# Kernel tuning notes

Measured on AMD Instinct MI355X. Metric: run time of the kernel, lower is better.

## Reference

```python
import jax, jax.numpy as jnp
import numpy as np

B, D, U = 4096, 1024, 1024

def cumax(a):
    # Faithful to source: softmax over last axis, cumsum over axis 0 (TF defaults).
    return jnp.cumsum(jax.nn.softmax(a, axis=-1), axis=0)

def setup_inputs() -> dict:
    key = jax.random.key(0)
    ks = jax.random.split(key, 21)
    names = ['inputs', 'hidden_prev', 'cell_prev',
             'Wf', 'Uf', 'bf', 'Wi', 'Ui', 'bi', 'Wo', 'Uo', 'bo',
             'Wc', 'Uc', 'bc', 'Wft', 'Uft', 'bft', 'Wit', 'Uit', 'bit']
    shapes = [(B, D), (B, U), (B, U)] + [(D, U), (U, U), (U,)] * 6
    scales = [1.0, 1.0, 1.0] + [0.05, 0.05, 0.05] * 6  # random_normal init ~ small stddev
    return {n: jax.random.normal(k, s, dtype=jnp.float32) * sc
            for n, k, s, sc in zip(names, ks, shapes, scales)}

def reference(inputs, hidden_prev, cell_prev,
              Wf, Uf, bf, Wi, Ui, bi, Wo, Uo, bo,
              Wc, Uc, bc, Wft, Uft, bft, Wit, Uit, bit):
    # Fuse the 12 small GEMMs into 2 big ones: [B,D]@[D,6U] and [B,U]@[U,6U]
    W_all = jnp.concatenate([Wf, Wi, Wo, Wc, Wft, Wit], axis=1)   # [D, 6U]
    U_all = jnp.concatenate([Uf, Ui, Uo, Uc, Uft, Uit], axis=1)   # [U, 6U]
    b_all = jnp.concatenate([bf, bi, bo, bc, bft, bit], axis=0)   # [6U]
    pre = inputs @ W_all + hidden_prev @ U_all + b_all            # [B, 6U]
    zf, zi, zo, zc, zft, zit = [pre[:, j*U:(j+1)*U] for j in range(6)]

    f = jax.nn.sigmoid(zf)
    i = jax.nn.sigmoid(zi)
    o = jax.nn.sigmoid(zo)
    c_hat = jnp.tanh(zc)
    f_tilde = cumax(zft)
    i_tilde = 1.0 - cumax(zit)

    omega = f_tilde * i_tilde
    f_hat = f * omega + (f_tilde - omega)
    i_hat = i * omega + (i_tilde - omega)
    cell = f_hat * cell_prev + i_hat * c_hat
    hidden = o * jnp.tanh(cell)
    return hidden, cell
```

## Files before the change

kernel.cpp:

```cpp
#include <hip/hip_runtime.h>
#include <cstdint>
#include <cstddef>


typedef _Float16 half8  __attribute__((ext_vector_type(8)));
typedef _Float16 half4v __attribute__((ext_vector_type(4)));
typedef float f32x4 __attribute__((ext_vector_type(4)));

__device__ __forceinline__ void async16(const _Float16* g, _Float16* l) {
  __builtin_amdgcn_global_load_lds(
      (const __attribute__((address_space(1))) void*)g,
      (__attribute__((address_space(3))) void*)l, 16, 0, 0);
}

struct Ptrs12 { const float* p[12]; };
struct Ptrs6  { const float* p[6];  };

__global__ void prep(const float* __restrict__ X, const float* __restrict__ H,
                     Ptrs12 w, Ptrs6 bs,
                     _Float16* __restrict__ Ahi, _Float16* __restrict__ Bhi,
                     float* __restrict__ b_all) {
  __shared__ float tile[64][65];
  const int blk = blockIdx.x;
  const int t = threadIdx.x;
  if (blk < 8192) {
    size_t base = ((size_t)blk * 256 + t) * 4;
    int k = (int)(base & 2047);
    size_t b = base >> 11;
    const float* src = (k < 1024) ? (X + b * 1024 + k) : (H + b * 1024 + (k - 1024));
    float4 v = *(const float4*)src;
    half4v hi = { (_Float16)v.x, (_Float16)v.y, (_Float16)v.z, (_Float16)v.w };
    *(half4v*)(Ahi + base) = hi;
  } else if (blk < 11264) {
    int bb = blk - 8192;
    int mat = bb >> 8;
    int tl = bb & 255;
    int tr = tl >> 4, tc = tl & 15;
    int g = mat >> 1, s = mat & 1;
    const float* src = w.p[mat];
    int col = t & 63, r0 = t >> 6;
#pragma unroll
    for (int i = 0; i < 16; i++) {
      int row = i * 4 + r0;
      tile[row][col] = src[(size_t)(tr * 64 + row) * 1024 + tc * 64 + col];
    }
    __syncthreads();
    int c2 = t >> 2, kseg = t & 3;
    half8 v0, v1;
#pragma unroll
    for (int j = 0; j < 8; j++) {
      v0[j] = (_Float16)(tile[kseg * 16 + j][c2] * 64.0f);
      v1[j] = (_Float16)(tile[kseg * 16 + 8 + j][c2] * 64.0f);
    }
    size_t n  = (size_t)g * 1024 + tc * 64 + c2;
    size_t kk = (size_t)s * 1024 + tr * 64 + kseg * 16;
    *(half8*)(Bhi + n * 2048 + kk) = v0;
    *(half8*)(Bhi + n * 2048 + kk + 8) = v1;
  } else {
    int n = (blk - 11264) * 256 + t;
    b_all[n] = bs.p[n >> 10][n & 1023];
  }
}


#define LGKM0 asm volatile("s_waitcnt lgkmcnt(0)" ::: "memory")

__device__ __forceinline__ void wg_barrier() {
  __builtin_amdgcn_s_barrier();
  asm volatile("" ::: "memory");
}

__global__ __launch_bounds__(512, 2) void gemm_ring(
    const _Float16* __restrict__ Ah, const _Float16* __restrict__ Bh,
    const float* __restrict__ b_all, _Float16* __restrict__ pre16) {
  __shared__ __attribute__((aligned(16))) _Float16 lds[73728];

  const int bid = blockIdx.x;
  const int swz = (bid & 7) * 96 + (bid >> 3);
  const int nTile = swz / 32;
  const int mTile = swz % 32;

  const int t = threadIdx.x;
  const int lane = t & 63;
  const int wave = t >> 6;
  const int wm = wave >> 2, wn = wave & 3;
  const int kgrp = lane >> 4, frow = lane & 15;

  const _Float16* Abase = Ah + (size_t)mTile * 128 * 2048;
  const _Float16* Bbase = Bh + (size_t)nTile * 256 * 2048;

  f32x4 acc[4][4] = {};

  auto stage_tile = [&](int kt, int base) {
#pragma unroll
    for (int q = 0; q < 2; q++) {
      int s = q * 512 + t;
      int r = s >> 3, k8 = s & 7;
      int xs = k8 ^ (r & 7);
      async16(Abase + (size_t)r * 2048 + kt * 64 + xs * 8, lds + base + s * 8);
    }
#pragma unroll
    for (int q = 0; q < 4; q++) {
      int s = q * 512 + t;
      int r = s >> 3, k8 = s & 7;
      int xs = k8 ^ (r & 7);
      async16(Bbase + (size_t)r * 2048 + kt * 64 + xs * 8,
              lds + base + 8192 + s * 8);
    }
  };

  int cur = 0, nxt = 24576, nn = 49152;

  stage_tile(0, cur);
  stage_tile(1, nxt);
  asm volatile("s_waitcnt vmcnt(6)" ::: "memory");
  wg_barrier();

  for (int T = 0; T < 32; T++) {
    const _Float16* A_ = lds + cur;
    const _Float16* B_ = lds + cur + 8192;
    half8 af[4][2], bf[4][2];
#pragma unroll
    for (int mi = 0; mi < 4; mi++) {
      int r = wm * 64 + mi * 16 + frow;
#pragma unroll
      for (int ks = 0; ks < 2; ks++)
        af[mi][ks] = *(const half8*)(A_ + r * 64 +
                                     (((ks * 4 + kgrp) ^ (r & 7)) * 8));
    }
#pragma unroll
    for (int nj = 0; nj < 4; nj++) {
      int r = wn * 64 + nj * 16 + frow;
#pragma unroll
      for (int ks = 0; ks < 2; ks++)
        bf[nj][ks] = *(const half8*)(B_ + r * 64 +
                                     (((ks * 4 + kgrp) ^ (r & 7)) * 8));
    }
    if (T + 2 < 32) stage_tile(T + 2, nn);

    __builtin_amdgcn_s_setprio(1);
#pragma unroll
    for (int mi = 0; mi < 4; mi++)
#pragma unroll
      for (int nj = 0; nj < 4; nj++)
        acc[mi][nj] = __builtin_amdgcn_mfma_f32_16x16x32_f16(
            af[mi][0], bf[nj][0], acc[mi][nj], 0, 0, 0);
    __builtin_amdgcn_s_setprio(0);

    LGKM0;
    if (T < 30) {
      asm volatile("s_waitcnt vmcnt(6)" ::: "memory");
      wg_barrier();
    } else if (T == 30) {
      asm volatile("s_waitcnt vmcnt(0)" ::: "memory");
      wg_barrier();
    }

    __builtin_amdgcn_s_setprio(1);
#pragma unroll
    for (int mi = 0; mi < 4; mi++)
#pragma unroll
      for (int nj = 0; nj < 4; nj++)
        acc[mi][nj] = __builtin_amdgcn_mfma_f32_16x16x32_f16(
            af[mi][1], bf[nj][1], acc[mi][nj], 0, 0, 0);
    __builtin_amdgcn_s_setprio(0);

    int tmp = cur; cur = nxt; nxt = nn; nn = tmp;
  }

  __syncthreads();
  const float inv64 = 1.0f / 64.0f;
  const int cb = nTile * 256;
  float bias[4];
#pragma unroll
  for (int nj = 0; nj < 4; nj++)
    bias[nj] = b_all[cb + wn * 64 + nj * 16 + frow];
#pragma unroll
  for (int mi = 0; mi < 4; mi++) {
#pragma unroll
    for (int nj = 0; nj < 4; nj++) {
      int row = wm * 64 + mi * 16 + kgrp * 4;
      int col = wn * 64 + nj * 16 + frow;
#pragma unroll
      for (int j = 0; j < 4; j++)
        lds[(row + j) * 264 + col] =
            (_Float16)(acc[mi][nj][j] * inv64 + bias[nj]);
    }
  }
  __syncthreads();
#pragma unroll
  for (int rr = 0; rr < 8; rr++) {
    int L = rr * 4096 + t * 8;
    int row = L >> 8, col = L & 255;
    half8 v = *(const half8*)(lds + row * 264 + col);
    *(half8*)(pre16 + (size_t)(mTile * 128 + row) * 6144 + cb + col) = v;
  }
}

__global__ void softmax_partials(_Float16* __restrict__ pre16, f32x4* __restrict__ part4) {
  __shared__ float wsum[4][1024];
  int m = blockIdx.x >> 10;
  int ch = blockIdx.x & 1023;
  int t = threadIdx.x;
  int wave = t >> 6, lane = t & 63;
  f32x4 colacc[4] = {};
  {
    int b = ch * 4 + wave;
    _Float16* row = pre16 + (size_t)b * 6144 + (4 + m) * 1024;
    f32x4 v[4];
    float mx = -3.4e38f;
#pragma unroll
    for (int j = 0; j < 4; j++) {
      half4v h = *(const half4v*)(row + lane * 4 + 256 * j);
      v[j] = f32x4{ (float)h[0], (float)h[1], (float)h[2], (float)h[3] };
      mx = fmaxf(mx, fmaxf(fmaxf(v[j][0], v[j][1]), fmaxf(v[j][2], v[j][3])));
    }
#pragma unroll
    for (int off = 32; off > 0; off >>= 1) mx = fmaxf(mx, __shfl_xor(mx, off, 64));
    float sum = 0.f;
#pragma unroll
    for (int j = 0; j < 4; j++)
#pragma unroll
      for (int q = 0; q < 4; q++) { v[j][q] = __expf(v[j][q] - mx); sum += v[j][q]; }
#pragma unroll
    for (int off = 32; off > 0; off >>= 1) sum += __shfl_xor(sum, off, 64);
    float inv = 1.f / sum;
#pragma unroll
    for (int j = 0; j < 4; j++) {
      v[j] *= inv;
      half4v h = { (_Float16)v[j][0], (_Float16)v[j][1], (_Float16)v[j][2], (_Float16)v[j][3] };
      *(half4v*)(row + lane * 4 + 256 * j) = h;
      colacc[j] += v[j];
    }
  }
#pragma unroll
  for (int j = 0; j < 4; j++)
    *(f32x4*)(&wsum[wave][lane * 4 + 256 * j]) = colacc[j];
  __syncthreads();
  f32x4 s = *(const f32x4*)(&wsum[0][t * 4]);
  s += *(const f32x4*)(&wsum[1][t * 4]);
  s += *(const f32x4*)(&wsum[2][t * 4]);
  s += *(const f32x4*)(&wsum[3][t * 4]);
  part4[((size_t)m * 256 + t) * 1024 + ch] = s;
}

__global__ void scan_partials(const f32x4* __restrict__ part4, f32x4* __restrict__ off4) {
  int gidx = blockIdx.x * 4 + (threadIdx.x >> 6);
  int lane = threadIdx.x & 63;
  size_t base = (size_t)gidx * 1024;
  f32x4 v[16];
  f32x4 s = {};
#pragma unroll
  for (int j = 0; j < 16; j++) {
    v[j] = part4[base + lane * 16 + j];
    s += v[j];
  }
  f32x4 incl = s;
#pragma unroll
  for (int off = 1; off < 64; off <<= 1) {
    f32x4 o;
#pragma unroll
    for (int q = 0; q < 4; q++) o[q] = __shfl_up(incl[q], off, 64);
    if (lane >= off) incl += o;
  }
  f32x4 run = incl - s;
#pragma unroll
  for (int j = 0; j < 16; j++) {
    off4[base + lane * 16 + j] = run;
    run += v[j];
  }
}

__device__ __forceinline__ float fast_sigmoid(float x) {
  return __builtin_amdgcn_rcpf(1.f + __expf(-x));
}
__device__ __forceinline__ float fast_tanh(float x) {
  float xc = fminf(fmaxf(x, -15.f), 15.f);
  float e = __expf(2.f * xc);
  return (e - 1.f) * __builtin_amdgcn_rcpf(e + 1.f);
}

__global__ void onlstm_final(const _Float16* __restrict__ pre16,
                             const float* __restrict__ cprev, const f32x4* __restrict__ off4,
                             float* __restrict__ out) {
  int ch = blockIdx.x;
  int c4 = threadIdx.x;
  int c = c4 * 4;
  f32x4 runf = off4[(size_t)c4 * 1024 + ch];
  f32x4 runi = off4[(size_t)(256 + c4) * 1024 + ch];
  for (int r = 0; r < 4; r++) {
    int b = ch * 4 + r;
    const _Float16* row = pre16 + (size_t)b * 6144;
    half4v zf = *(const half4v*)(row + c);
    half4v zi = *(const half4v*)(row + 1024 + c);
    half4v zo = *(const half4v*)(row + 2048 + c);
    half4v zc = *(const half4v*)(row + 3072 + c);
    half4v pf = *(const half4v*)(row + 4096 + c);
    half4v pi = *(const half4v*)(row + 5120 + c);
    f32x4 cp = *(const f32x4*)(cprev + (size_t)b * 1024 + c);
    f32x4 hid, cel;
#pragma unroll
    for (int q = 0; q < 4; q++) {
      runf[q] += (float)pf[q];
      runi[q] += (float)pi[q];
      float ft = runf[q], it = 1.f - runi[q];
      float f  = fast_sigmoid((float)zf[q]);
      float ii = fast_sigmoid((float)zi[q]);
      float o  = fast_sigmoid((float)zo[q]);
      float chat = fast_tanh((float)zc[q]);
      float omega = ft * it;
      float fhat = f * omega + (ft - omega);
      float ihat = ii * omega + (it - omega);
      float cell = fhat * cp[q] + ihat * chat;
      hid[q] = o * fast_tanh(cell);
      cel[q] = cell;
    }
    *(f32x4*)(out + (size_t)b * 1024 + c) = hid;
    *(f32x4*)(out + (size_t)4194304 + (size_t)b * 1024 + c) = cel;
  }
}

extern "C" void kernel_launch(void* const* d_in, const int* in_sizes, int n_in,
                              void* d_out, int out_size, void* d_ws, size_t ws_size,
                              hipStream_t stream) {
  const float* X = (const float*)d_in[0];
  const float* H = (const float*)d_in[1];
  const float* C = (const float*)d_in[2];

  char* ws = (char*)d_ws;
  _Float16* pre16 = (_Float16*)(ws);
  _Float16* Ahi   = (_Float16*)(ws + 50331648);
  _Float16* Bhi   = (_Float16*)(ws + 67108864);
  float*    b_all = (float*)(ws + 92274688);
  f32x4*    part4 = (f32x4*)(ws + 50331648);
  f32x4*    off4  = (f32x4*)(ws + 58720256);

  Ptrs12 w;
  for (int g = 0; g < 6; g++) {
    w.p[2 * g]     = (const float*)d_in[3 + 3 * g];
    w.p[2 * g + 1] = (const float*)d_in[4 + 3 * g];
  }
  Ptrs6 bs;
  for (int g = 0; g < 6; g++) bs.p[g] = (const float*)d_in[5 + 3 * g];

  prep<<<11288, 256, 0, stream>>>(X, H, w, bs, Ahi, Bhi, b_all);
  gemm_ring<<<768, 512, 0, stream>>>(Ahi, Bhi, b_all, pre16);
  softmax_partials<<<2048, 256, 0, stream>>>(pre16, part4);
  scan_partials<<<128, 256, 0, stream>>>(part4, off4);
  onlstm_final<<<1024, 256, 0, stream>>>(pre16, C, off4, (float*)d_out);
}
```

Baseline: 316.3 us.

## Fuse softmax, scan and final gating into one cooperative kernel with grid sync

Replaces the three tail kernels (softmax partials, partial scan, final elementwise) with a single cooperative kernel of 512 blocks that uses grid.sync between phases. Each block handles 8 rows and keeps the normalized softmax probabilities in LDS instead of writing them back to global and re-reading them, and the scan is restructured to one block per column group. This removes two launches and a global round-trip of the softmax output. In exchange it adds two grid-wide barriers, and the 8-row batch with a 48KB LDS footprint could lower occupancy.

```diff
diff --git a/kernel.cpp b/kernel.cpp
--- a/kernel.cpp
+++ b/kernel.cpp
@@ -1,6 +1,9 @@
 #include <hip/hip_runtime.h>
+#include <hip/hip_cooperative_groups.h>
 #include <cstdint>
 #include <cstddef>
+
+namespace cg = cooperative_groups;
 
 
 typedef _Float16 half8  __attribute__((ext_vector_type(8)));
@@ -197,79 +200,6 @@
   }
 }
 
-__global__ void softmax_partials(_Float16* __restrict__ pre16, f32x4* __restrict__ part4) {
-  __shared__ float wsum[4][1024];
-  int m = blockIdx.x >> 10;
-  int ch = blockIdx.x & 1023;
-  int t = threadIdx.x;
-  int wave = t >> 6, lane = t & 63;
-  f32x4 colacc[4] = {};
-  {
-    int b = ch * 4 + wave;
-    _Float16* row = pre16 + (size_t)b * 6144 + (4 + m) * 1024;
-    f32x4 v[4];
-    float mx = -3.4e38f;
-#pragma unroll
-    for (int j = 0; j < 4; j++) {
-      half4v h = *(const half4v*)(row + lane * 4 + 256 * j);
-      v[j] = f32x4{ (float)h[0], (float)h[1], (float)h[2], (float)h[3] };
-      mx = fmaxf(mx, fmaxf(fmaxf(v[j][0], v[j][1]), fmaxf(v[j][2], v[j][3])));
-    }
-#pragma unroll
-    for (int off = 32; off > 0; off >>= 1) mx = fmaxf(mx, __shfl_xor(mx, off, 64));
-    float sum = 0.f;
-#pragma unroll
-    for (int j = 0; j < 4; j++)
-#pragma unroll
-      for (int q = 0; q < 4; q++) { v[j][q] = __expf(v[j][q] - mx); sum += v[j][q]; }
-#pragma unroll
-    for (int off = 32; off > 0; off >>= 1) sum += __shfl_xor(sum, off, 64);
-    float inv = 1.f / sum;
-#pragma unroll
-    for (int j = 0; j < 4; j++) {
-      v[j] *= inv;
-      half4v h = { (_Float16)v[j][0], (_Float16)v[j][1], (_Float16)v[j][2], (_Float16)v[j][3] };
-      *(half4v*)(row + lane * 4 + 256 * j) = h;
-      colacc[j] += v[j];
-    }
-  }
-#pragma unroll
-  for (int j = 0; j < 4; j++)
-    *(f32x4*)(&wsum[wave][lane * 4 + 256 * j]) = colacc[j];
-  __syncthreads();
-  f32x4 s = *(const f32x4*)(&wsum[0][t * 4]);
-  s += *(const f32x4*)(&wsum[1][t * 4]);
-  s += *(const f32x4*)(&wsum[2][t * 4]);
-  s += *(const f32x4*)(&wsum[3][t * 4]);
-  part4[((size_t)m * 256 + t) * 1024 + ch] = s;
-}
-
-__global__ void scan_partials(const f32x4* __restrict__ part4, f32x4* __restrict__ off4) {
-  int gidx = blockIdx.x * 4 + (threadIdx.x >> 6);
-  int lane = threadIdx.x & 63;
-  size_t base = (size_t)gidx * 1024;
-  f32x4 v[16];
-  f32x4 s = {};
-#pragma unroll
-  for (int j = 0; j < 16; j++) {
-    v[j] = part4[base + lane * 16 + j];
-    s += v[j];
-  }
-  f32x4 incl = s;
-#pragma unroll
-  for (int off = 1; off < 64; off <<= 1) {
-    f32x4 o;
-#pragma unroll
-    for (int q = 0; q < 4; q++) o[q] = __shfl_up(incl[q], off, 64);
-    if (lane >= off) incl += o;
-  }
-  f32x4 run = incl - s;
-#pragma unroll
-  for (int j = 0; j < 16; j++) {
-    off4[base + lane * 16 + j] = run;
-    run += v[j];
-  }
-}
 
 __device__ __forceinline__ float fast_sigmoid(float x) {
   return __builtin_amdgcn_rcpf(1.f + __expf(-x));
@@ -280,43 +210,133 @@
   return (e - 1.f) * __builtin_amdgcn_rcpf(e + 1.f);
 }
 
-__global__ void onlstm_final(const _Float16* __restrict__ pre16,
-                             const float* __restrict__ cprev, const f32x4* __restrict__ off4,
-                             float* __restrict__ out) {
-  int ch = blockIdx.x;
-  int c4 = threadIdx.x;
-  int c = c4 * 4;
-  f32x4 runf = off4[(size_t)c4 * 1024 + ch];
-  f32x4 runi = off4[(size_t)(256 + c4) * 1024 + ch];
-  for (int r = 0; r < 4; r++) {
-    int b = ch * 4 + r;
-    const _Float16* row = pre16 + (size_t)b * 6144;
-    half4v zf = *(const half4v*)(row + c);
-    half4v zi = *(const half4v*)(row + 1024 + c);
-    half4v zo = *(const half4v*)(row + 2048 + c);
-    half4v zc = *(const half4v*)(row + 3072 + c);
-    half4v pf = *(const half4v*)(row + 4096 + c);
-    half4v pi = *(const half4v*)(row + 5120 + c);
-    f32x4 cp = *(const f32x4*)(cprev + (size_t)b * 1024 + c);
-    f32x4 hid, cel;
-#pragma unroll
-    for (int q = 0; q < 4; q++) {
-      runf[q] += (float)pf[q];
-      runi[q] += (float)pi[q];
-      float ft = runf[q], it = 1.f - runi[q];
-      float f  = fast_sigmoid((float)zf[q]);
-      float ii = fast_sigmoid((float)zi[q]);
-      float o  = fast_sigmoid((float)zo[q]);
-      float chat = fast_tanh((float)zc[q]);
-      float omega = ft * it;
-      float fhat = f * omega + (ft - omega);
-      float ihat = ii * omega + (it - omega);
-      float cell = fhat * cp[q] + ihat * chat;
-      hid[q] = o * fast_tanh(cell);
-      cel[q] = cell;
-    }
-    *(f32x4*)(out + (size_t)b * 1024 + c) = hid;
-    *(f32x4*)(out + (size_t)4194304 + (size_t)b * 1024 + c) = cel;
+__global__ __launch_bounds__(256) void fused_tail(
+    const _Float16* __restrict__ pre16, const float* __restrict__ cprev,
+    f32x4* __restrict__ part4, f32x4* __restrict__ off4,
+    float* __restrict__ out) {
+  __shared__ _Float16 p_lds[8 * 2048];
+  __shared__ float wsum[4][1024];
+  __shared__ f32x4 wtot[4];
+
+  cg::grid_group grid = cg::this_grid();
+
+  const int ch = blockIdx.x;
+  const int t = threadIdx.x;
+  const int wave = t >> 6, lane = t & 63;
+
+#pragma unroll
+  for (int m = 0; m < 2; m++) {
+    f32x4 colacc[4] = {};
+#pragma unroll
+    for (int rr = 0; rr < 2; rr++) {
+      int rloc = wave * 2 + rr;
+      int b = ch * 8 + rloc;
+      const _Float16* row = pre16 + (size_t)b * 6144 + (4 + m) * 1024;
+      f32x4 v[4];
+      float mx = -3.4e38f;
+#pragma unroll
+      for (int j = 0; j < 4; j++) {
+        half4v h = *(const half4v*)(row + lane * 4 + 256 * j);
+        v[j] = f32x4{ (float)h[0], (float)h[1], (float)h[2], (float)h[3] };
+        mx = fmaxf(mx, fmaxf(fmaxf(v[j][0], v[j][1]), fmaxf(v[j][2], v[j][3])));
+      }
+#pragma unroll
+      for (int off = 32; off > 0; off >>= 1) mx = fmaxf(mx, __shfl_xor(mx, off, 64));
+      float sum = 0.f;
+#pragma unroll
+      for (int j = 0; j < 4; j++)
+#pragma unroll
+        for (int q = 0; q < 4; q++) { v[j][q] = __expf(v[j][q] - mx); sum += v[j][q]; }
+#pragma unroll
+      for (int off = 32; off > 0; off >>= 1) sum += __shfl_xor(sum, off, 64);
+      float inv = 1.f / sum;
+#pragma unroll
+      for (int j = 0; j < 4; j++) {
+        v[j] *= inv;
+        half4v h = { (_Float16)v[j][0], (_Float16)v[j][1],
+                     (_Float16)v[j][2], (_Float16)v[j][3] };
+        *(half4v*)(&p_lds[rloc * 2048 + m * 1024 + lane * 4 + 256 * j]) = h;
+        colacc[j] += v[j];
+      }
+    }
+#pragma unroll
+    for (int j = 0; j < 4; j++)
+      *(f32x4*)(&wsum[wave][lane * 4 + 256 * j]) = colacc[j];
+    __syncthreads();
+    f32x4 s = *(const f32x4*)(&wsum[0][t * 4]);
+    s += *(const f32x4*)(&wsum[1][t * 4]);
+    s += *(const f32x4*)(&wsum[2][t * 4]);
+    s += *(const f32x4*)(&wsum[3][t * 4]);
+    part4[((size_t)m * 256 + t) * 512 + ch] = s;
+    __syncthreads();
+  }
+
+  __threadfence();
+  grid.sync();
+  __threadfence();
+
+  {
+    const int g = ch;
+    f32x4 e0 = part4[(size_t)g * 512 + 2 * t];
+    f32x4 e1 = part4[(size_t)g * 512 + 2 * t + 1];
+    f32x4 ps = e0 + e1;
+    f32x4 incl = ps;
+#pragma unroll
+    for (int off = 1; off < 64; off <<= 1) {
+      f32x4 o;
+#pragma unroll
+      for (int q = 0; q < 4; q++) o[q] = __shfl_up(incl[q], off, 64);
+      if (lane >= off) incl += o;
+    }
+    if (lane == 63) wtot[wave] = incl;
+    __syncthreads();
+    f32x4 woff = {};
+#pragma unroll
+    for (int w = 0; w < 4; w++)
+      if (w < wave) woff += wtot[w];
+    f32x4 excl = woff + incl - ps;
+    off4[(size_t)g * 512 + 2 * t] = excl;
+    off4[(size_t)g * 512 + 2 * t + 1] = excl + e0;
+  }
+
+  __threadfence();
+  grid.sync();
+  __threadfence();
+
+  {
+    const int c4 = t, c = t * 4;
+    f32x4 runf = off4[(size_t)c4 * 512 + ch];
+    f32x4 runi = off4[(size_t)(256 + c4) * 512 + ch];
+    for (int r = 0; r < 8; r++) {
+      int b = ch * 8 + r;
+      const _Float16* row = pre16 + (size_t)b * 6144;
+      half4v zf = *(const half4v*)(row + c);
+      half4v zi = *(const half4v*)(row + 1024 + c);
+      half4v zo = *(const half4v*)(row + 2048 + c);
+      half4v zc = *(const half4v*)(row + 3072 + c);
+      half4v pf = *(const half4v*)(&p_lds[r * 2048 + c]);
+      half4v pi = *(const half4v*)(&p_lds[r * 2048 + 1024 + c]);
+      f32x4 cp = *(const f32x4*)(cprev + (size_t)b * 1024 + c);
+      f32x4 hid, cel;
+#pragma unroll
+      for (int q = 0; q < 4; q++) {
+        runf[q] += (float)pf[q];
+        runi[q] += (float)pi[q];
+        float ft = runf[q], it = 1.f - runi[q];
+        float f  = fast_sigmoid((float)zf[q]);
+        float ii = fast_sigmoid((float)zi[q]);
+        float o  = fast_sigmoid((float)zo[q]);
+        float chat = fast_tanh((float)zc[q]);
+        float omega = ft * it;
+        float fhat = f * omega + (ft - omega);
+        float ihat = ii * omega + (it - omega);
+        float cell = fhat * cp[q] + ihat * chat;
+        hid[q] = o * fast_tanh(cell);
+        cel[q] = cell;
+      }
+      *(f32x4*)(out + (size_t)b * 1024 + c) = hid;
+      *(f32x4*)(out + (size_t)4194304 + (size_t)b * 1024 + c) = cel;
+    }
   }
 }
 
@@ -333,7 +353,7 @@
   _Float16* Bhi   = (_Float16*)(ws + 67108864);
   float*    b_all = (float*)(ws + 92274688);
   f32x4*    part4 = (f32x4*)(ws + 50331648);
-  f32x4*    off4  = (f32x4*)(ws + 58720256);
+  f32x4*    off4  = (f32x4*)(ws + 54525952);
 
   Ptrs12 w;
   for (int g = 0; g < 6; g++) {
@@ -345,7 +365,11 @@
 
   prep<<<11288, 256, 0, stream>>>(X, H, w, bs, Ahi, Bhi, b_all);
   gemm_ring<<<768, 512, 0, stream>>>(Ahi, Bhi, b_all, pre16);
-  softmax_partials<<<2048, 256, 0, stream>>>(pre16, part4);
-  scan_partials<<<128, 256, 0, stream>>>(part4, off4);
-  onlstm_final<<<1024, 256, 0, stream>>>(pre16, C, off4, (float*)d_out);
-}
+
+  const _Float16* pre16c = pre16;
+  float* outp = (float*)d_out;
+  void* args[5] = { (void*)&pre16c, (void*)&C, (void*)&part4,
+                    (void*)&off4, (void*)&outp };
+  hipLaunchCooperativeKernel((const void*)fused_tail, dim3(512), dim3(256),
+                             args, 0, stream);
+}
```

Measured after the change: 620.1 us. +96.0%, slower.
